# Kernel tuning notes

Measured on AMD Instinct MI355X. Metric: run time of the kernel, lower is better.

## Reference

```python
import jax, jax.numpy as jnp
import numpy as np

NEG_SLOPE = 0.2


def setup_inputs() -> dict:
    key = jax.random.key(0)
    k1, k2, k3, k4, k5 = jax.random.split(key, 5)
    N, D, E = 10000, 128, 640000
    feat = jax.random.normal(k1, (N, D), dtype=jnp.float32)
    # nn.Linear weight [out_feats, in_feats]; scale like default init
    fc_weight = jax.random.normal(k2, (D, D), dtype=jnp.float32) / jnp.sqrt(jnp.float32(D))
    attn = jax.random.normal(k3, (1, 1, D), dtype=jnp.float32) * 0.1
    eps = jnp.zeros((1,), dtype=jnp.float32)
    src = jax.random.randint(k4, (E,), 0, N, dtype=jnp.int32)
    dst = jax.random.randint(k5, (E,), 0, N, dtype=jnp.int32)
    return {"feat": feat, "fc_weight": fc_weight, "attn": attn, "eps": eps,
            "src": src, "dst": dst}


def reference(feat, fc_weight, attn, eps, src, dst):
    N = feat.shape[0]
    # --- get_attention_tensor (attn_type='MX', num_heads=1) ---
    proj = feat @ fc_weight.T                      # [N, out]
    el = proj[src]                                  # [E, out] u side
    er = proj[dst]                                  # [E, out] v side
    a = attn.reshape(-1)                            # [out]
    e = jnp.sum(jax.nn.leaky_relu(el + er, NEG_SLOPE) * a, axis=-1)   # [E]
    gate = jax.nn.sigmoid(jnp.sum(el * er, axis=-1))                  # [E] sigmoid(u_dot_v)
    w = jax.nn.sigmoid(e * gate)                    # [E] final per-edge weight
    # --- message passing: u_mul_e('h','_edge_weight') with 'mean' reduce ---
    msg = feat[src] * w[:, None]                    # [E, D]
    neigh_sum = jax.ops.segment_sum(msg, dst, num_segments=N)         # [N, D]
    deg = jax.ops.segment_sum(jnp.ones_like(w), dst, num_segments=N)  # [N]
    neigh = neigh_sum / jnp.maximum(deg, 1.0)[:, None]                # mean; 0 for deg-0
    # --- node update ---
    rst = (1.0 + eps[0]) * feat + neigh
    return rst
```

## Files before the change

### kernel.cpp

```cpp
#include <hip/hip_runtime.h>

#define DD 128
#define CAP 128
#define BH 128

typedef unsigned short ushort_t;
typedef __attribute__((ext_vector_type(8))) short bf16x8;
typedef __attribute__((ext_vector_type(4))) float f32x4;

__device__ __forceinline__ unsigned short f2bf(float f) {
    unsigned u = __float_as_uint(f);
    u = (u + 0x7FFFu + ((u >> 16) & 1u)) >> 16;
    return (unsigned short)u;
}
__device__ __forceinline__ float bflo(unsigned v) { return __uint_as_float(v << 16); }
__device__ __forceinline__ float bfhi(unsigned v) { return __uint_as_float(v & 0xFFFF0000u); }
__device__ __forceinline__ unsigned pack2(float a, float b) {
    return (unsigned)f2bf(a) | ((unsigned)f2bf(b) << 16);
}
__device__ __forceinline__ bf16x8 cvt8(const float* __restrict__ p) {
    float4 f0 = *(const float4*)p;
    float4 f1 = *(const float4*)(p + 4);
    bf16x8 v;
    v[0] = (short)f2bf(f0.x); v[1] = (short)f2bf(f0.y);
    v[2] = (short)f2bf(f0.z); v[3] = (short)f2bf(f0.w);
    v[4] = (short)f2bf(f1.x); v[5] = (short)f2bf(f1.y);
    v[6] = (short)f2bf(f1.z); v[7] = (short)f2bf(f1.w);
    return v;
}

__global__ __launch_bounds__(256) void k1_hist_gemm(
    const float* __restrict__ feat, const float* __restrict__ W,
    const float* __restrict__ attn, const int* __restrict__ dst,
    ushort_t* __restrict__ projb, float* __restrict__ dotA,
    ushort_t* __restrict__ cnt, unsigned char* __restrict__ rank8,
    int N, int E, int CE)
{
    extern __shared__ unsigned h[];
    int b = (int)blockIdx.x;
    if (b < BH) {
        int NW = (N + 1) >> 1;
        for (int i = threadIdx.x; i < NW; i += 256) h[i] = 0;
        __syncthreads();
        int base = b * CE;
        for (int k = threadIdx.x; k < CE; k += 256) {
            int i = base + k;
            if (i < E) {
                int d = dst[i];
                unsigned r = atomicAdd(&h[d >> 1], (d & 1) ? 0x10000u : 1u);
                r = (r >> ((d & 1) * 16)) & 0xFFFFu;
                rank8[i] = (unsigned char)(r > 255u ? 255u : r);
            }
        }
        __syncthreads();
        ushort_t* crow = cnt + (size_t)b * N;
        for (int i = threadIdx.x; i < N; i += 256)
            crow[i] = (ushort_t)((h[i >> 1] >> ((i & 1) * 16)) & 0xFFFFu);
        return;
    }
    int rowTile = (b - BH) * 4 + ((int)threadIdx.x >> 6);
    if (rowTile * 16 >= N) return;
    int lane = threadIdx.x & 63;
    int m = lane & 15;
    int quad = lane >> 4;
    const float* arow = feat + (size_t)(rowTile * 16 + m) * DD + quad * 8;
    bf16x8 afr[4];
#pragma unroll
    for (int ks = 0; ks < 4; ++ks) afr[ks] = cvt8(arow + ks * 32);
    float dacc0 = 0.f, dacc1 = 0.f, dacc2 = 0.f, dacc3 = 0.f;
#pragma unroll
    for (int ct = 0; ct < 8; ++ct) {
        const float* brow = W + (size_t)(ct * 16 + m) * DD + quad * 8;
        f32x4 acc = {0.f, 0.f, 0.f, 0.f};
#pragma unroll
        for (int ks = 0; ks < 4; ++ks) {
            bf16x8 bb = cvt8(brow + ks * 32);
            acc = __builtin_amdgcn_mfma_f32_16x16x32_bf16(afr[ks], bb, acc, 0, 0, 0);
        }
        ushort_t* orow = projb + (size_t)(rowTile * 16 + quad * 4) * DD
                       + ct * 16 + m;
#pragma unroll
        for (int r = 0; r < 4; ++r)
            orow[(size_t)r * DD] = f2bf(acc[r]);
        float av = 0.6f * attn[ct * 16 + m];
        dacc0 = fmaf(av, acc[0], dacc0);
        dacc1 = fmaf(av, acc[1], dacc1);
        dacc2 = fmaf(av, acc[2], dacc2);
        dacc3 = fmaf(av, acc[3], dacc3);
    }
#pragma unroll
    for (int o = 1; o < 16; o <<= 1) {
        dacc0 += __shfl_xor(dacc0, o); dacc1 += __shfl_xor(dacc1, o);
        dacc2 += __shfl_xor(dacc2, o); dacc3 += __shfl_xor(dacc3, o);
    }
    if (m == 0) {
        int rbase = rowTile * 16 + quad * 4;
        if (rbase + 3 < N) {
            dotA[rbase]     = dacc0;
            dotA[rbase + 1] = dacc1;
            dotA[rbase + 2] = dacc2;
            dotA[rbase + 3] = dacc3;
        }
    }
}

__global__ __launch_bounds__(256) void k2_scan_cast(
    const float* __restrict__ feat, const ushort_t* __restrict__ cnt,
    ushort_t* __restrict__ offs, int* __restrict__ totals,
    ushort_t* __restrict__ featb, int N, int SC)
{
    int b = (int)blockIdx.x;
    if (b < SC) {
        int bin = b * 256 + (int)threadIdx.x;
        if (bin >= N) return;
        int run = 0;
#pragma unroll 8
        for (int blk = 0; blk < BH; ++blk) {
            int v = cnt[(size_t)blk * N + bin];
            offs[(size_t)blk * N + bin] = (ushort_t)run;
            run += v;
        }
        totals[bin] = run;
        return;
    }
    size_t total = (size_t)N * DD;
    size_t idx = ((size_t)(b - SC) * 256 + threadIdx.x) * 8;
    if (idx + 7 < total) {
        float4 f0 = *(const float4*)(feat + idx);
        float4 f1 = *(const float4*)(feat + idx + 4);
        uint4 o;
        o.x = pack2(f0.x, f0.y); o.y = pack2(f0.z, f0.w);
        o.z = pack2(f1.x, f1.y); o.w = pack2(f1.z, f1.w);
        *(uint4*)(featb + idx) = o;
    } else {
        for (size_t i = idx; i < total; ++i) featb[i] = f2bf(feat[i]);
    }
}

__global__ __launch_bounds__(256) void k3_scatter(
    const int* __restrict__ src, const int* __restrict__ dst,
    const unsigned char* __restrict__ rank8, const ushort_t* __restrict__ offs,
    ushort_t* __restrict__ sorted, int N, int E, int CE)
{
    int t = ((int)blockIdx.x * 256 + (int)threadIdx.x) * 4;
    if (t + 3 < E) {
        int4 s4 = *(const int4*)(src + t);
        int4 d4 = *(const int4*)(dst + t);
        uchar4 r4 = *(const uchar4*)(rank8 + t);
        int b0 = t / CE, b3 = (t + 3) / CE;
        int b1 = (t + 1) / CE, b2 = (t + 2) / CE;
        unsigned p0 = (unsigned)offs[(size_t)b0 * N + d4.x] + r4.x;
        unsigned p1 = (unsigned)offs[(size_t)b1 * N + d4.y] + r4.y;
        unsigned p2 = (unsigned)offs[(size_t)b2 * N + d4.z] + r4.z;
        unsigned p3 = (unsigned)offs[(size_t)b3 * N + d4.w] + r4.w;
        if (p0 < CAP) sorted[(size_t)d4.x * CAP + p0] = (ushort_t)s4.x;
        if (p1 < CAP) sorted[(size_t)d4.y * CAP + p1] = (ushort_t)s4.y;
        if (p2 < CAP) sorted[(size_t)d4.z * CAP + p2] = (ushort_t)s4.z;
        if (p3 < CAP) sorted[(size_t)d4.w * CAP + p3] = (ushort_t)s4.w;
    } else {
        for (int q = 0; q < 4; ++q) {
            int i = t + q;
            if (i < E) {
                int d = dst[i];
                unsigned pos = (unsigned)offs[(size_t)(i / CE) * N + d] + rank8[i];
                if (pos < CAP) sorted[(size_t)d * CAP + pos] = (ushort_t)src[i];
            }
        }
    }
}

__global__ __launch_bounds__(256) void seg_agg(
    const ushort_t* __restrict__ projb, const ushort_t* __restrict__ featb,
    const float* __restrict__ feat, const float* __restrict__ attn,
    const float* __restrict__ dotA, const ushort_t* __restrict__ sorted,
    const int* __restrict__ totals, const float* __restrict__ eps,
    float* __restrict__ out, int N)
{
    int wid = (int)((blockIdx.x * (size_t)blockDim.x + threadIdx.x) >> 6);
    if (wid >= N) return;
    int lane = threadIdx.x & 63;
    int g   = lane >> 3;
    int sub = lane & 7;

    const uint4* projv = (const uint4*)projb;
    const uint4* featv = (const uint4*)featb;

    int m = min(totals[wid], CAP);
    const ushort_t* lst = sorted + (size_t)wid * CAP;

    uint4 ev0 = projv[(size_t)wid * 16 + 2 * sub];
    uint4 ev1 = projv[(size_t)wid * 16 + 2 * sub + 1];
    float er[16] = {
        bflo(ev0.x), bfhi(ev0.x), bflo(ev0.y), bfhi(ev0.y),
        bflo(ev0.z), bfhi(ev0.z), bflo(ev0.w), bfhi(ev0.w),
        bflo(ev1.x), bfhi(ev1.x), bflo(ev1.y), bfhi(ev1.y),
        bflo(ev1.z), bfhi(ev1.z), bflo(ev1.w), bfhi(ev1.w)};
    float av[16];
#pragma unroll
    for (int k = 0; k < 16; ++k) av[k] = 0.4f * attn[16 * sub + k];
    float dAr = dotA[wid];
    float c[16];
#pragma unroll
    for (int k = 0; k < 16; ++k) c[k] = 0.f;

    uint4 apv0, apv1, afv0, afv1; float adAl = 0.f;
    uint4 bpv0, bpv1, bfv0, bfv1; float bdAl = 0.f;

    auto ldst = [&](int idx, uint4& pv0, uint4& pv1, uint4& fv0, uint4& fv1,
                    float& dAl) {
        int s = (idx < m) ? (int)lst[idx] : 0;
        pv0 = projv[(size_t)s * 16 + 2 * sub];
        pv1 = projv[(size_t)s * 16 + 2 * sub + 1];
        fv0 = featv[(size_t)s * 16 + 2 * sub];
        fv1 = featv[(size_t)s * 16 + 2 * sub + 1];
        dAl = dotA[s];
    };

    int i = g;
    if (i < m)     ldst(i,     apv0, apv1, afv0, afv1, adAl);
    if (i + 8 < m) ldst(i + 8, bpv0, bpv1, bfv0, bfv1, bdAl);

    while (i < m) {
        uint4 cpv0, cpv1, cfv0, cfv1; float cdAl;
        ldst(i + 16, cpv0, cpv1, cfv0, cfv1, cdAl);
        float el[16] = {
            bflo(apv0.x), bfhi(apv0.x), bflo(apv0.y), bfhi(apv0.y),
            bflo(apv0.z), bfhi(apv0.z), bflo(apv0.w), bfhi(apv0.w),
            bflo(apv1.x), bfhi(apv1.x), bflo(apv1.y), bfhi(apv1.y),
            bflo(apv1.z), bfhi(apv1.z), bflo(apv1.w), bfhi(apv1.w)};
        float gp = 0.f, ad = 0.f;
#pragma unroll
        for (int k = 0; k < 16; ++k) {
            gp = fmaf(el[k], er[k], gp);
            ad = fmaf(fabsf(el[k] + er[k]), av[k], ad);
        }
#pragma unroll
        for (int o = 1; o <= 4; o <<= 1) {
            gp += __shfl_xor(gp, o);
            ad += __shfl_xor(ad, o);
        }
        float ep = adAl + dAr + ad;
        float gate = 1.f / (1.f + __expf(-gp));
        float w = 1.f / (1.f + __expf(-ep * gate));
        float fl[16] = {
            bflo(afv0.x), bfhi(afv0.x), bflo(afv0.y), bfhi(afv0.y),
            bflo(afv0.z), bfhi(afv0.z), bflo(afv0.w), bfhi(afv0.w),
            bflo(afv1.x), bfhi(afv1.x), bflo(afv1.y), bfhi(afv1.y),
            bflo(afv1.z), bfhi(afv1.z), bflo(afv1.w), bfhi(afv1.w)};
#pragma unroll
        for (int k = 0; k < 16; ++k) c[k] = fmaf(fl[k], w, c[k]);
        apv0 = bpv0; apv1 = bpv1; afv0 = bfv0; afv1 = bfv1; adAl = bdAl;
        bpv0 = cpv0; bpv1 = cpv1; bfv0 = cfv0; bfv1 = cfv1; bdAl = cdAl;
        i += 8;
    }
#pragma unroll
    for (int o = 8; o <= 32; o <<= 1) {
#pragma unroll
        for (int k = 0; k < 16; ++k) c[k] += __shfl_xor(c[k], o);
    }
    if (g == 0) {
        float inv = 1.f / fmaxf((float)m, 1.f);
        float sc = 1.f + eps[0];
        const f32x4* fsrc = (const f32x4*)feat + (size_t)wid * 32 + 4 * sub;
        f32x4* od = (f32x4*)out + (size_t)wid * 32 + 4 * sub;
#pragma unroll
        for (int q = 0; q < 4; ++q) {
            f32x4 f = __builtin_nontemporal_load(&fsrc[q]);
            f32x4 o;
            o[0] = fmaf(sc, f[0], c[4 * q] * inv);
            o[1] = fmaf(sc, f[1], c[4 * q + 1] * inv);
            o[2] = fmaf(sc, f[2], c[4 * q + 2] * inv);
            o[3] = fmaf(sc, f[3], c[4 * q + 3] * inv);
            __builtin_nontemporal_store(o, &od[q]);
        }
    }
}

extern "C" void kernel_launch(void* const* d_in, const int* in_sizes, int n_in,
                              void* d_out, int out_size, void* d_ws, size_t ws_size,
                              hipStream_t stream) {
    const float* feat = (const float*)d_in[0];
    const float* W    = (const float*)d_in[1];
    const float* attn = (const float*)d_in[2];
    const float* eps  = (const float*)d_in[3];
    const int*   src  = (const int*)d_in[4];
    const int*   dst  = (const int*)d_in[5];
    int N = in_sizes[0] / DD;
    int E = in_sizes[4];

    ushort_t* projb  = (ushort_t*)d_ws;
    ushort_t* featb  = projb + (size_t)N * DD;
    ushort_t* sorted = featb + (size_t)N * DD;
    ushort_t* cnt    = sorted + (size_t)N * CAP;
    ushort_t* offs   = cnt + (size_t)BH * N;
    int*      totals = (int*)(offs + (size_t)BH * N);
    float*    dotA   = (float*)(totals + N);
    unsigned char* rank8 = (unsigned char*)(dotA + N);

    int CE = (E + BH - 1) / BH;
    int GB = ((N + 15) / 16 + 3) / 4;
    int SC = (N + 255) / 256;
    int CB = (N * DD + 2047) / 2048;
    int SB = (E / 4 + 255) / 256 + 1;
    size_t ldsB = (size_t)((N + 1) / 2) * sizeof(unsigned);

    k1_hist_gemm<<<BH + GB, 256, ldsB, stream>>>(
        feat, W, attn, dst, projb, dotA, cnt, rank8, N, E, CE);
    k2_scan_cast<<<SC + CB, 256, 0, stream>>>(
        feat, cnt, offs, totals, featb, N, SC);
    k3_scatter<<<SB, 256, 0, stream>>>(src, dst, rank8, offs, sorted, N, E, CE);
    seg_agg<<<(N * 64 + 255) / 256, 256, 0, stream>>>(
        projb, featb, feat, attn, dotA, sorted, totals, eps,
        (float*)d_out, N);
}
```

Measured before the change: 138.1 us.

## Compute per-edge weights in scatter kernel and pack with source index

The per-edge attention weight is now computed in the scatter kernel, in edge order, by gathering both endpoint projections. The weight is stored as bf16 packed next to the 16-bit source index in a 32-bit sorted entry. The aggregation kernel then only gathers source features and no longer loads projections or computes attention. This moves the projection gathers out of the latency-bound aggregation loop. In exchange the scatter kernel does two random projection gathers per edge, the sorted buffer doubles in size, and the weight is rounded to bf16.

```diff
diff --git a/kernel.cpp b/kernel.cpp
--- a/kernel.cpp
+++ b/kernel.cpp
@@ -137,44 +137,66 @@
     }
 }
 
-__global__ __launch_bounds__(256) void k3_scatter(
+__global__ __launch_bounds__(256) void k3_weight_scatter(
     const int* __restrict__ src, const int* __restrict__ dst,
     const unsigned char* __restrict__ rank8, const ushort_t* __restrict__ offs,
-    ushort_t* __restrict__ sorted, int N, int E, int CE)
+    const ushort_t* __restrict__ projb, const float* __restrict__ dotA,
+    const float* __restrict__ attn, unsigned* __restrict__ swsorted,
+    int N, int E, int CE)
 {
-    int t = ((int)blockIdx.x * 256 + (int)threadIdx.x) * 4;
-    if (t + 3 < E) {
-        int4 s4 = *(const int4*)(src + t);
-        int4 d4 = *(const int4*)(dst + t);
-        uchar4 r4 = *(const uchar4*)(rank8 + t);
-        int b0 = t / CE, b3 = (t + 3) / CE;
-        int b1 = (t + 1) / CE, b2 = (t + 2) / CE;
-        unsigned p0 = (unsigned)offs[(size_t)b0 * N + d4.x] + r4.x;
-        unsigned p1 = (unsigned)offs[(size_t)b1 * N + d4.y] + r4.y;
-        unsigned p2 = (unsigned)offs[(size_t)b2 * N + d4.z] + r4.z;
-        unsigned p3 = (unsigned)offs[(size_t)b3 * N + d4.w] + r4.w;
-        if (p0 < CAP) sorted[(size_t)d4.x * CAP + p0] = (ushort_t)s4.x;
-        if (p1 < CAP) sorted[(size_t)d4.y * CAP + p1] = (ushort_t)s4.y;
-        if (p2 < CAP) sorted[(size_t)d4.z * CAP + p2] = (ushort_t)s4.z;
-        if (p3 < CAP) sorted[(size_t)d4.w * CAP + p3] = (ushort_t)s4.w;
-    } else {
-        for (int q = 0; q < 4; ++q) {
-            int i = t + q;
-            if (i < E) {
-                int d = dst[i];
-                unsigned pos = (unsigned)offs[(size_t)(i / CE) * N + d] + rank8[i];
-                if (pos < CAP) sorted[(size_t)d * CAP + pos] = (ushort_t)src[i];
-            }
+    int sub = (int)threadIdx.x & 7;
+    int gidx = (int)threadIdx.x >> 3;
+    const uint4* pv = (const uint4*)projb;
+    float av[16];
+#pragma unroll
+    for (int k = 0; k < 16; ++k) av[k] = 0.4f * attn[16 * sub + k];
+    int base = (int)blockIdx.x * 128;
+#pragma unroll
+    for (int q = 0; q < 4; ++q) {
+        int e = base + q * 32 + gidx;
+        int ee = (e < E) ? e : 0;
+        int s = src[ee], d = dst[ee];
+        uint4 a0 = pv[(size_t)s * 16 + 2 * sub];
+        uint4 a1 = pv[(size_t)s * 16 + 2 * sub + 1];
+        uint4 b0 = pv[(size_t)d * 16 + 2 * sub];
+        uint4 b1 = pv[(size_t)d * 16 + 2 * sub + 1];
+        float el[16] = {
+            bflo(a0.x), bfhi(a0.x), bflo(a0.y), bfhi(a0.y),
+            bflo(a0.z), bfhi(a0.z), bflo(a0.w), bfhi(a0.w),
+            bflo(a1.x), bfhi(a1.x), bflo(a1.y), bfhi(a1.y),
+            bflo(a1.z), bfhi(a1.z), bflo(a1.w), bfhi(a1.w)};
+        float er[16] = {
+            bflo(b0.x), bfhi(b0.x), bflo(b0.y), bfhi(b0.y),
+            bflo(b0.z), bfhi(b0.z), bflo(b0.w), bfhi(b0.w),
+            bflo(b1.x), bfhi(b1.x), bflo(b1.y), bfhi(b1.y),
+            bflo(b1.z), bfhi(b1.z), bflo(b1.w), bfhi(b1.w)};
+        float gp = 0.f, ad = 0.f;
+#pragma unroll
+        for (int k = 0; k < 16; ++k) {
+            gp = fmaf(el[k], er[k], gp);
+            ad = fmaf(fabsf(el[k] + er[k]), av[k], ad);
+        }
+#pragma unroll
+        for (int o = 1; o <= 4; o <<= 1) {
+            gp += __shfl_xor(gp, o);
+            ad += __shfl_xor(ad, o);
+        }
+        if (sub == 0 && e < E) {
+            float ep = dotA[s] + dotA[d] + ad;
+            float gate = 1.f / (1.f + __expf(-gp));
+            float w = 1.f / (1.f + __expf(-ep * gate));
+            unsigned pos = (unsigned)offs[(size_t)(e / CE) * N + d] + rank8[e];
+            if (pos < CAP)
+                swsorted[(size_t)d * CAP + pos] =
+                    (unsigned)s | ((unsigned)f2bf(w) << 16);
         }
     }
 }
 
 __global__ __launch_bounds__(256) void seg_agg(
-    const ushort_t* __restrict__ projb, const ushort_t* __restrict__ featb,
-    const float* __restrict__ feat, const float* __restrict__ attn,
-    const float* __restrict__ dotA, const ushort_t* __restrict__ sorted,
-    const int* __restrict__ totals, const float* __restrict__ eps,
-    float* __restrict__ out, int N)
+    const ushort_t* __restrict__ featb, const float* __restrict__ feat,
+    const unsigned* __restrict__ swsorted, const int* __restrict__ totals,
+    const float* __restrict__ eps, float* __restrict__ out, int N)
 {
     int wid = (int)((blockIdx.x * (size_t)blockDim.x + threadIdx.x) >> 6);
     if (wid >= N) return;
@@ -182,75 +204,41 @@
     int g   = lane >> 3;
     int sub = lane & 7;
 
-    const uint4* projv = (const uint4*)projb;
-    const uint4* featv = (const uint4*)featb;
-
+    const uint4* fv = (const uint4*)featb;
     int m = min(totals[wid], CAP);
-    const ushort_t* lst = sorted + (size_t)wid * CAP;
-
-    uint4 ev0 = projv[(size_t)wid * 16 + 2 * sub];
-    uint4 ev1 = projv[(size_t)wid * 16 + 2 * sub + 1];
-    float er[16] = {
-        bflo(ev0.x), bfhi(ev0.x), bflo(ev0.y), bfhi(ev0.y),
-        bflo(ev0.z), bfhi(ev0.z), bflo(ev0.w), bfhi(ev0.w),
-        bflo(ev1.x), bfhi(ev1.x), bflo(ev1.y), bfhi(ev1.y),
-        bflo(ev1.z), bfhi(ev1.z), bflo(ev1.w), bfhi(ev1.w)};
-    float av[16];
-#pragma unroll
-    for (int k = 0; k < 16; ++k) av[k] = 0.4f * attn[16 * sub + k];
-    float dAr = dotA[wid];
+    const unsigned* swl = swsorted + (size_t)wid * CAP;
+
     float c[16];
 #pragma unroll
     for (int k = 0; k < 16; ++k) c[k] = 0.f;
 
-    uint4 apv0, apv1, afv0, afv1; float adAl = 0.f;
-    uint4 bpv0, bpv1, bfv0, bfv1; float bdAl = 0.f;
-
-    auto ldst = [&](int idx, uint4& pv0, uint4& pv1, uint4& fv0, uint4& fv1,
-                    float& dAl) {
-        int s = (idx < m) ? (int)lst[idx] : 0;
-        pv0 = projv[(size_t)s * 16 + 2 * sub];
-        pv1 = projv[(size_t)s * 16 + 2 * sub + 1];
-        fv0 = featv[(size_t)s * 16 + 2 * sub];
-        fv1 = featv[(size_t)s * 16 + 2 * sub + 1];
-        dAl = dotA[s];
+    unsigned swA = 0; uint4 fA0, fA1;
+    unsigned swB = 0; uint4 fB0, fB1;
+    auto ldst = [&](int idx, unsigned& sw, uint4& f0, uint4& f1) {
+        unsigned v = (idx < m) ? swl[idx] : 0u;
+        sw = v;
+        int s = (int)(v & 0xFFFFu);
+        f0 = fv[(size_t)s * 16 + 2 * sub];
+        f1 = fv[(size_t)s * 16 + 2 * sub + 1];
     };
 
     int i = g;
-    if (i < m)     ldst(i,     apv0, apv1, afv0, afv1, adAl);
-    if (i + 8 < m) ldst(i + 8, bpv0, bpv1, bfv0, bfv1, bdAl);
+    if (i < m)     ldst(i,     swA, fA0, fA1);
+    if (i + 8 < m) ldst(i + 8, swB, fB0, fB1);
 
     while (i < m) {
-        uint4 cpv0, cpv1, cfv0, cfv1; float cdAl;
-        ldst(i + 16, cpv0, cpv1, cfv0, cfv1, cdAl);
-        float el[16] = {
-            bflo(apv0.x), bfhi(apv0.x), bflo(apv0.y), bfhi(apv0.y),
-            bflo(apv0.z), bfhi(apv0.z), bflo(apv0.w), bfhi(apv0.w),
-            bflo(apv1.x), bfhi(apv1.x), bflo(apv1.y), bfhi(apv1.y),
-            bflo(apv1.z), bfhi(apv1.z), bflo(apv1.w), bfhi(apv1.w)};
-        float gp = 0.f, ad = 0.f;
-#pragma unroll
-        for (int k = 0; k < 16; ++k) {
-            gp = fmaf(el[k], er[k], gp);
-            ad = fmaf(fabsf(el[k] + er[k]), av[k], ad);
-        }
-#pragma unroll
-        for (int o = 1; o <= 4; o <<= 1) {
-            gp += __shfl_xor(gp, o);
-            ad += __shfl_xor(ad, o);
-        }
-        float ep = adAl + dAr + ad;
-        float gate = 1.f / (1.f + __expf(-gp));
-        float w = 1.f / (1.f + __expf(-ep * gate));
+        unsigned swC; uint4 fC0, fC1;
+        ldst(i + 16, swC, fC0, fC1);
+        float w = bfhi(swA);
         float fl[16] = {
-            bflo(afv0.x), bfhi(afv0.x), bflo(afv0.y), bfhi(afv0.y),
-            bflo(afv0.z), bfhi(afv0.z), bflo(afv0.w), bfhi(afv0.w),
-            bflo(afv1.x), bfhi(afv1.x), bflo(afv1.y), bfhi(afv1.y),
-            bflo(afv1.z), bfhi(afv1.z), bflo(afv1.w), bfhi(afv1.w)};
+            bflo(fA0.x), bfhi(fA0.x), bflo(fA0.y), bfhi(fA0.y),
+            bflo(fA0.z), bfhi(fA0.z), bflo(fA0.w), bfhi(fA0.w),
+            bflo(fA1.x), bfhi(fA1.x), bflo(fA1.y), bfhi(fA1.y),
+            bflo(fA1.z), bfhi(fA1.z), bflo(fA1.w), bfhi(fA1.w)};
 #pragma unroll
         for (int k = 0; k < 16; ++k) c[k] = fmaf(fl[k], w, c[k]);
-        apv0 = bpv0; apv1 = bpv1; afv0 = bfv0; afv1 = bfv1; adAl = bdAl;
-        bpv0 = cpv0; bpv1 = cpv1; bfv0 = cfv0; bfv1 = cfv1; bdAl = cdAl;
+        swA = swB; fA0 = fB0; fA1 = fB1;
+        swB = swC; fB0 = fC0; fB1 = fC1;
         i += 8;
     }
 #pragma unroll
@@ -290,8 +278,8 @@
 
     ushort_t* projb  = (ushort_t*)d_ws;
     ushort_t* featb  = projb + (size_t)N * DD;
-    ushort_t* sorted = featb + (size_t)N * DD;
-    ushort_t* cnt    = sorted + (size_t)N * CAP;
+    unsigned* swsorted = (unsigned*)(featb + (size_t)N * DD);
+    ushort_t* cnt    = (ushort_t*)(swsorted + (size_t)N * CAP);
     ushort_t* offs   = cnt + (size_t)BH * N;
     int*      totals = (int*)(offs + (size_t)BH * N);
     float*    dotA   = (float*)(totals + N);
@@ -301,15 +289,15 @@
     int GB = ((N + 15) / 16 + 3) / 4;
     int SC = (N + 255) / 256;
     int CB = (N * DD + 2047) / 2048;
-    int SB = (E / 4 + 255) / 256 + 1;
+    int WB = (E + 127) / 128;
     size_t ldsB = (size_t)((N + 1) / 2) * sizeof(unsigned);
 
     k1_hist_gemm<<<BH + GB, 256, ldsB, stream>>>(
         feat, W, attn, dst, projb, dotA, cnt, rank8, N, E, CE);
     k2_scan_cast<<<SC + CB, 256, 0, stream>>>(
         feat, cnt, offs, totals, featb, N, SC);
-    k3_scatter<<<SB, 256, 0, stream>>>(src, dst, rank8, offs, sorted, N, E, CE);
+    k3_weight_scatter<<<WB, 256, 0, stream>>>(
+        src, dst, rank8, offs, projb, dotA, attn, swsorted, N, E, CE);
     seg_agg<<<(N * 64 + 255) / 256, 256, 0, stream>>>(
-        projb, featb, feat, attn, dotA, sorted, totals, eps,
-        (float*)d_out, N);
-}
+        featb, feat, swsorted, totals, eps, (float*)d_out, N);
+}
```

Result: slower. 142.3 us (+3.0%).

## Fuse cast into hist/GEMM kernel and compute prefix offsets in scatter blocks

Applied to the files above, without the earlier changes.

Merges the bf16 feature cast into the first kernel alongside the histogram and projection GEMM, and removes the separate scan kernel. Each scatter block now rebuilds its per-chunk prefix offsets in LDS by summing earlier histogram rows, and extra blocks compute per-node totals. The histogram chunk count drops from 128 to 32, which shrinks the count array and the redundant prefix work. This saves one launch and the offs array round trip, but the later scatter blocks must read up to 31 count rows each, and fewer histogram blocks means less parallelism in that phase.

```diff
diff --git a/kernel.cpp b/kernel.cpp
--- a/kernel.cpp
+++ b/kernel.cpp
@@ -2,7 +2,7 @@
 
 #define DD 128
 #define CAP 128
-#define BH 128
+#define BH 32
 
 typedef unsigned short ushort_t;
 typedef __attribute__((ext_vector_type(8))) short bf16x8;
@@ -29,12 +29,12 @@
     return v;
 }
 
-__global__ __launch_bounds__(256) void k1_hist_gemm(
+__global__ __launch_bounds__(256) void kA_hist_gemm_cast(
     const float* __restrict__ feat, const float* __restrict__ W,
     const float* __restrict__ attn, const int* __restrict__ dst,
     ushort_t* __restrict__ projb, float* __restrict__ dotA,
-    ushort_t* __restrict__ cnt, unsigned char* __restrict__ rank8,
-    int N, int E, int CE)
+    ushort_t* __restrict__ featb, ushort_t* __restrict__ cnt,
+    unsigned char* __restrict__ rank8, int N, int E, int CE, int GB)
 {
     extern __shared__ unsigned h[];
     int b = (int)blockIdx.x;
@@ -43,14 +43,12 @@
         for (int i = threadIdx.x; i < NW; i += 256) h[i] = 0;
         __syncthreads();
         int base = b * CE;
-        for (int k = threadIdx.x; k < CE; k += 256) {
-            int i = base + k;
-            if (i < E) {
-                int d = dst[i];
-                unsigned r = atomicAdd(&h[d >> 1], (d & 1) ? 0x10000u : 1u);
-                r = (r >> ((d & 1) * 16)) & 0xFFFFu;
-                rank8[i] = (unsigned char)(r > 255u ? 255u : r);
-            }
+        int hi = min(base + CE, E);
+        for (int k = base + (int)threadIdx.x; k < hi; k += 256) {
+            int d = dst[k];
+            unsigned r = atomicAdd(&h[d >> 1], (d & 1) ? 0x10000u : 1u);
+            r = (r >> ((d & 1) * 16)) & 0xFFFFu;
+            rank8[k] = (unsigned char)(r > 255u ? 255u : r);
         }
         __syncthreads();
         ushort_t* crow = cnt + (size_t)b * N;
@@ -58,73 +56,55 @@
             crow[i] = (ushort_t)((h[i >> 1] >> ((i & 1) * 16)) & 0xFFFFu);
         return;
     }
-    int rowTile = (b - BH) * 4 + ((int)threadIdx.x >> 6);
-    if (rowTile * 16 >= N) return;
-    int lane = threadIdx.x & 63;
-    int m = lane & 15;
-    int quad = lane >> 4;
-    const float* arow = feat + (size_t)(rowTile * 16 + m) * DD + quad * 8;
-    bf16x8 afr[4];
-#pragma unroll
-    for (int ks = 0; ks < 4; ++ks) afr[ks] = cvt8(arow + ks * 32);
-    float dacc0 = 0.f, dacc1 = 0.f, dacc2 = 0.f, dacc3 = 0.f;
-#pragma unroll
-    for (int ct = 0; ct < 8; ++ct) {
-        const float* brow = W + (size_t)(ct * 16 + m) * DD + quad * 8;
-        f32x4 acc = {0.f, 0.f, 0.f, 0.f};
-#pragma unroll
-        for (int ks = 0; ks < 4; ++ks) {
-            bf16x8 bb = cvt8(brow + ks * 32);
-            acc = __builtin_amdgcn_mfma_f32_16x16x32_bf16(afr[ks], bb, acc, 0, 0, 0);
-        }
-        ushort_t* orow = projb + (size_t)(rowTile * 16 + quad * 4) * DD
-                       + ct * 16 + m;
-#pragma unroll
-        for (int r = 0; r < 4; ++r)
-            orow[(size_t)r * DD] = f2bf(acc[r]);
-        float av = 0.6f * attn[ct * 16 + m];
-        dacc0 = fmaf(av, acc[0], dacc0);
-        dacc1 = fmaf(av, acc[1], dacc1);
-        dacc2 = fmaf(av, acc[2], dacc2);
-        dacc3 = fmaf(av, acc[3], dacc3);
-    }
-#pragma unroll
-    for (int o = 1; o < 16; o <<= 1) {
-        dacc0 += __shfl_xor(dacc0, o); dacc1 += __shfl_xor(dacc1, o);
-        dacc2 += __shfl_xor(dacc2, o); dacc3 += __shfl_xor(dacc3, o);
-    }
-    if (m == 0) {
-        int rbase = rowTile * 16 + quad * 4;
-        if (rbase + 3 < N) {
-            dotA[rbase]     = dacc0;
-            dotA[rbase + 1] = dacc1;
-            dotA[rbase + 2] = dacc2;
-            dotA[rbase + 3] = dacc3;
-        }
-    }
-}
-
-__global__ __launch_bounds__(256) void k2_scan_cast(
-    const float* __restrict__ feat, const ushort_t* __restrict__ cnt,
-    ushort_t* __restrict__ offs, int* __restrict__ totals,
-    ushort_t* __restrict__ featb, int N, int SC)
-{
-    int b = (int)blockIdx.x;
-    if (b < SC) {
-        int bin = b * 256 + (int)threadIdx.x;
-        if (bin >= N) return;
-        int run = 0;
-#pragma unroll 8
-        for (int blk = 0; blk < BH; ++blk) {
-            int v = cnt[(size_t)blk * N + bin];
-            offs[(size_t)blk * N + bin] = (ushort_t)run;
-            run += v;
-        }
-        totals[bin] = run;
+    if (b < BH + GB) {
+        int rowTile = (b - BH) * 4 + ((int)threadIdx.x >> 6);
+        if (rowTile * 16 >= N) return;
+        int lane = threadIdx.x & 63;
+        int m = lane & 15;
+        int quad = lane >> 4;
+        const float* arow = feat + (size_t)(rowTile * 16 + m) * DD + quad * 8;
+        bf16x8 afr[4];
+#pragma unroll
+        for (int ks = 0; ks < 4; ++ks) afr[ks] = cvt8(arow + ks * 32);
+        float dacc0 = 0.f, dacc1 = 0.f, dacc2 = 0.f, dacc3 = 0.f;
+#pragma unroll
+        for (int ct = 0; ct < 8; ++ct) {
+            const float* brow = W + (size_t)(ct * 16 + m) * DD + quad * 8;
+            f32x4 acc = {0.f, 0.f, 0.f, 0.f};
+#pragma unroll
+            for (int ks = 0; ks < 4; ++ks) {
+                bf16x8 bb = cvt8(brow + ks * 32);
+                acc = __builtin_amdgcn_mfma_f32_16x16x32_bf16(afr[ks], bb, acc, 0, 0, 0);
+            }
+            ushort_t* orow = projb + (size_t)(rowTile * 16 + quad * 4) * DD
+                           + ct * 16 + m;
+#pragma unroll
+            for (int r = 0; r < 4; ++r)
+                orow[(size_t)r * DD] = f2bf(acc[r]);
+            float av = 0.6f * attn[ct * 16 + m];
+            dacc0 = fmaf(av, acc[0], dacc0);
+            dacc1 = fmaf(av, acc[1], dacc1);
+            dacc2 = fmaf(av, acc[2], dacc2);
+            dacc3 = fmaf(av, acc[3], dacc3);
+        }
+#pragma unroll
+        for (int o = 1; o < 16; o <<= 1) {
+            dacc0 += __shfl_xor(dacc0, o); dacc1 += __shfl_xor(dacc1, o);
+            dacc2 += __shfl_xor(dacc2, o); dacc3 += __shfl_xor(dacc3, o);
+        }
+        if (m == 0) {
+            int rbase = rowTile * 16 + quad * 4;
+            if (rbase + 3 < N) {
+                dotA[rbase]     = dacc0;
+                dotA[rbase + 1] = dacc1;
+                dotA[rbase + 2] = dacc2;
+                dotA[rbase + 3] = dacc3;
+            }
+        }
         return;
     }
     size_t total = (size_t)N * DD;
-    size_t idx = ((size_t)(b - SC) * 256 + threadIdx.x) * 8;
+    size_t idx = ((size_t)(b - BH - GB) * 256 + threadIdx.x) * 8;
     if (idx + 7 < total) {
         float4 f0 = *(const float4*)(feat + idx);
         float4 f1 = *(const float4*)(feat + idx + 4);
@@ -137,39 +117,63 @@
     }
 }
 
-__global__ __launch_bounds__(256) void k3_scatter(
+__global__ __launch_bounds__(256) void kB_scatter_totals(
     const int* __restrict__ src, const int* __restrict__ dst,
-    const unsigned char* __restrict__ rank8, const ushort_t* __restrict__ offs,
-    ushort_t* __restrict__ sorted, int N, int E, int CE)
+    const unsigned char* __restrict__ rank8, const ushort_t* __restrict__ cnt,
+    ushort_t* __restrict__ sorted, int* __restrict__ totals,
+    int N, int E, int CE, int SB)
 {
-    int t = ((int)blockIdx.x * 256 + (int)threadIdx.x) * 4;
-    if (t + 3 < E) {
-        int4 s4 = *(const int4*)(src + t);
-        int4 d4 = *(const int4*)(dst + t);
-        uchar4 r4 = *(const uchar4*)(rank8 + t);
-        int b0 = t / CE, b3 = (t + 3) / CE;
-        int b1 = (t + 1) / CE, b2 = (t + 2) / CE;
-        unsigned p0 = (unsigned)offs[(size_t)b0 * N + d4.x] + r4.x;
-        unsigned p1 = (unsigned)offs[(size_t)b1 * N + d4.y] + r4.y;
-        unsigned p2 = (unsigned)offs[(size_t)b2 * N + d4.z] + r4.z;
-        unsigned p3 = (unsigned)offs[(size_t)b3 * N + d4.w] + r4.w;
-        if (p0 < CAP) sorted[(size_t)d4.x * CAP + p0] = (ushort_t)s4.x;
-        if (p1 < CAP) sorted[(size_t)d4.y * CAP + p1] = (ushort_t)s4.y;
-        if (p2 < CAP) sorted[(size_t)d4.z * CAP + p2] = (ushort_t)s4.z;
-        if (p3 < CAP) sorted[(size_t)d4.w * CAP + p3] = (ushort_t)s4.w;
-    } else {
-        for (int q = 0; q < 4; ++q) {
-            int i = t + q;
-            if (i < E) {
-                int d = dst[i];
-                unsigned pos = (unsigned)offs[(size_t)(i / CE) * N + d] + rank8[i];
-                if (pos < CAP) sorted[(size_t)d * CAP + pos] = (ushort_t)src[i];
+    extern __shared__ unsigned p[];
+    int b = (int)blockIdx.x;
+    if (b < SB) {
+        int c = b >> 2, q = b & 3;
+        int NW = (N + 1) >> 1;
+        for (int i = threadIdx.x; i < NW; i += 256) p[i] = 0;
+        __syncthreads();
+        int NP = N >> 1;
+        for (int r = 0; r < c; ++r) {
+            const unsigned* row = (const unsigned*)(cnt + (size_t)r * N);
+            for (int i = threadIdx.x; i < NP; i += 256) p[i] += row[i];
+            if ((N & 1) && threadIdx.x == 0)
+                p[NP] += (unsigned)cnt[(size_t)r * N + (N - 1)];
+        }
+        __syncthreads();
+        int QE = CE >> 2;
+        int lo = c * CE + q * QE;
+        int hi = min(lo + QE, E);
+        for (int k = lo + (int)threadIdx.x * 4; k < hi; k += 1024) {
+            if (k + 3 < hi) {
+                int4 s4 = *(const int4*)(src + k);
+                int4 d4 = *(const int4*)(dst + k);
+                uchar4 r4 = *(const uchar4*)(rank8 + k);
+                unsigned p0 = ((p[d4.x >> 1] >> ((d4.x & 1) * 16)) & 0xFFFFu) + r4.x;
+                unsigned p1 = ((p[d4.y >> 1] >> ((d4.y & 1) * 16)) & 0xFFFFu) + r4.y;
+                unsigned p2 = ((p[d4.z >> 1] >> ((d4.z & 1) * 16)) & 0xFFFFu) + r4.z;
+                unsigned p3 = ((p[d4.w >> 1] >> ((d4.w & 1) * 16)) & 0xFFFFu) + r4.w;
+                if (p0 < CAP) sorted[(size_t)d4.x * CAP + p0] = (ushort_t)s4.x;
+                if (p1 < CAP) sorted[(size_t)d4.y * CAP + p1] = (ushort_t)s4.y;
+                if (p2 < CAP) sorted[(size_t)d4.z * CAP + p2] = (ushort_t)s4.z;
+                if (p3 < CAP) sorted[(size_t)d4.w * CAP + p3] = (ushort_t)s4.w;
+            } else {
+                for (int t = k; t < hi; ++t) {
+                    int d = dst[t];
+                    unsigned pos = ((p[d >> 1] >> ((d & 1) * 16)) & 0xFFFFu)
+                                 + rank8[t];
+                    if (pos < CAP) sorted[(size_t)d * CAP + pos] = (ushort_t)src[t];
+                }
             }
         }
-    }
-}
-
-__global__ __launch_bounds__(256) void seg_agg(
+        return;
+    }
+    int bin = (b - SB) * 256 + (int)threadIdx.x;
+    if (bin >= N) return;
+    int run = 0;
+#pragma unroll
+    for (int r = 0; r < BH; ++r) run += cnt[(size_t)r * N + bin];
+    totals[bin] = run;
+}
+
+__global__ __launch_bounds__(256) void kC_seg_agg(
     const ushort_t* __restrict__ projb, const ushort_t* __restrict__ featb,
     const float* __restrict__ feat, const float* __restrict__ attn,
     const float* __restrict__ dotA, const ushort_t* __restrict__ sorted,
@@ -292,24 +296,22 @@
     ushort_t* featb  = projb + (size_t)N * DD;
     ushort_t* sorted = featb + (size_t)N * DD;
     ushort_t* cnt    = sorted + (size_t)N * CAP;
-    ushort_t* offs   = cnt + (size_t)BH * N;
-    int*      totals = (int*)(offs + (size_t)BH * N);
+    int*      totals = (int*)(cnt + (size_t)BH * N);
     float*    dotA   = (float*)(totals + N);
     unsigned char* rank8 = (unsigned char*)(dotA + N);
 
-    int CE = (E + BH - 1) / BH;
+    int CE = (((E + BH - 1) / BH) + 15) & ~15;
     int GB = ((N + 15) / 16 + 3) / 4;
-    int SC = (N + 255) / 256;
     int CB = (N * DD + 2047) / 2048;
-    int SB = (E / 4 + 255) / 256 + 1;
-    size_t ldsB = (size_t)((N + 1) / 2) * sizeof(unsigned);
-
-    k1_hist_gemm<<<BH + GB, 256, ldsB, stream>>>(
-        feat, W, attn, dst, projb, dotA, cnt, rank8, N, E, CE);
-    k2_scan_cast<<<SC + CB, 256, 0, stream>>>(
-        feat, cnt, offs, totals, featb, N, SC);
-    k3_scatter<<<SB, 256, 0, stream>>>(src, dst, rank8, offs, sorted, N, E, CE);
-    seg_agg<<<(N * 64 + 255) / 256, 256, 0, stream>>>(
+    int SB = BH * 4;
+    int TB = (N + 255) / 256;
+    size_t ldsB = (size_t)((N + 1) / 2 + 1) * sizeof(unsigned);
+
+    kA_hist_gemm_cast<<<BH + GB + CB, 256, ldsB, stream>>>(
+        feat, W, attn, dst, projb, dotA, featb, cnt, rank8, N, E, CE, GB);
+    kB_scatter_totals<<<SB + TB, 256, ldsB, stream>>>(
+        src, dst, rank8, cnt, sorted, totals, N, E, CE, SB);
+    kC_seg_agg<<<(N * 64 + 255) / 256, 256, 0, stream>>>(
         projb, featb, feat, attn, dotA, sorted, totals, eps,
         (float*)d_out, N);
 }
```

Measured after the change: 182.4 us. +32.1%, slower.
